# Kernel optimization log

Hardware: AMD Instinct MI355X
Metric: run time of the kernel (lower is better)

Reference implementation:

```python
import jax, jax.numpy as jnp
import numpy as np

TEMPERATURE = 0.07
EPS = 1e-8  # torch CosineSimilarity eps


def setup_inputs() -> dict:
    key = jax.random.key(0)
    k1, k2, k3 = jax.random.split(key, 3)
    N, D = 8192, 512
    features = jax.random.normal(k1, (N, D), dtype=jnp.float32)
    positive_mask = jax.random.randint(k2, (N, N), 0, 2, dtype=jnp.int32)
    negative_mask = jax.random.randint(k3, (N, N), 0, 2, dtype=jnp.int32)
    return {"features": features, "positive_mask": positive_mask, "negative_mask": negative_mask}


def reference(features, positive_mask, negative_mask):
    N = positive_mask.shape[0]
    self_contrast = 1.0 - jnp.eye(N, dtype=features.dtype)  # zero diagonal
    pos = positive_mask.astype(features.dtype) * self_contrast  # [N, N]
    neg = negative_mask.astype(features.dtype) * self_contrast  # [N, N]

    # cosine similarity via normalized matmul (same math as broadcasted CosineSimilarity)
    norm = jnp.maximum(jnp.linalg.norm(features, axis=1, keepdims=True), EPS)
    fn = features / norm  # [N, D]
    sim = jnp.matmul(fn, fn.T) / TEMPERATURE  # [N, N]

    logits_max = jax.lax.stop_gradient(jnp.max(sim, axis=1, keepdims=True))
    e = jnp.exp(sim - logits_max)  # [N, N]

    positives = e * pos
    log_neg_sum = jnp.log(jnp.sum(e * neg, axis=1, keepdims=True))  # [N, 1]
    log_prob = positives - log_neg_sum  # [N, N] (faithful to source: exp-masked, not log)

    cardinal = jnp.sum(pos, axis=1)
    cardinal = jnp.where(cardinal == 0, 1.0, cardinal)
    log_prob_sum = jnp.sum(log_prob * pos, axis=1)
    loss = -log_prob_sum / cardinal
    return jnp.mean(loss)
```

## Files before the change

### kernel.cpp

```cpp
#include <hip/hip_runtime.h>
#include <hip/hip_bf16.h>
#include <math.h>

#define NN 8192
#define DD 512
#define INV_T 14.285714285714286f

typedef __attribute__((ext_vector_type(8))) short s16x8;
typedef __attribute__((ext_vector_type(4))) float f32x4;
typedef __attribute__((ext_vector_type(4))) int   i32x4;

__device__ __forceinline__ unsigned short f32_to_bf16(float f) {
  unsigned int u = __float_as_uint(f);
  u += 0x7FFFu + ((u >> 16) & 1u);
  return (unsigned short)(u >> 16);
}

__device__ __forceinline__ void async16(const void* g, void* l) {
  __builtin_amdgcn_global_load_lds((__attribute__((address_space(1))) void*)(void*)g,
                                   (__attribute__((address_space(3))) void*)l,
                                   16, 0, 0);
}

__global__ __launch_bounds__(256) void normalize_kernel(const float* __restrict__ f,
                                                        unsigned short* __restrict__ fnb) {
  const int wave = threadIdx.x >> 6;
  const int lane = threadIdx.x & 63;
  const int row  = blockIdx.x * 4 + wave;
  const float* src = f + (size_t)row * DD + lane * 8;
  float4 v0 = *(const float4*)src;
  float4 v1 = *(const float4*)(src + 4);
  float ss = v0.x*v0.x + v0.y*v0.y + v0.z*v0.z + v0.w*v0.w
           + v1.x*v1.x + v1.y*v1.y + v1.z*v1.z + v1.w*v1.w;
  #pragma unroll
  for (int o = 32; o; o >>= 1) ss += __shfl_xor(ss, o);
  const float r = 1.0f / fmaxf(sqrtf(ss), 1e-8f);
  ushort4 a, b;
  a.x = f32_to_bf16(v0.x * r); a.y = f32_to_bf16(v0.y * r);
  a.z = f32_to_bf16(v0.z * r); a.w = f32_to_bf16(v0.w * r);
  b.x = f32_to_bf16(v1.x * r); b.y = f32_to_bf16(v1.y * r);
  b.z = f32_to_bf16(v1.z * r); b.w = f32_to_bf16(v1.w * r);
  unsigned short* dst = fnb + (size_t)row * DD + lane * 8;
  *(ushort4*)dst = a;
  *(ushort4*)(dst + 4) = b;
}

__global__ __launch_bounds__(256, 3) void fused_kernel(const unsigned short* __restrict__ fnb,
                                                       const int* __restrict__ posm,
                                                       const int* __restrict__ negm,
                                                       float* __restrict__ Spos,
                                                       float* __restrict__ Sneg,
                                                       float* __restrict__ Pcnt) {
  const int bid = blockIdx.x;
  int bi = (int)(64.5 - sqrt(64.5 * 64.5 - 2.0 * (double)bid));
  while (64 * bi - bi * (bi - 1) / 2 > bid) --bi;
  while (64 * (bi + 1) - (bi + 1) * bi / 2 <= bid) ++bi;
  const int bj = bi + (bid - (64 * bi - bi * (bi - 1) / 2));
  const int I = bi * 128;
  const int J = bj * 128;
  const bool offdiag = (bi != bj);

  const int tid  = threadIdx.x;
  const int wave = tid >> 6;
  const int lane = tid & 63;
  const int wm = wave >> 1;
  const int wn = wave & 1;
  const int q   = lane >> 4;
  const int c16 = lane & 15;

  __shared__ alignas(16) unsigned short lA[128 * 32];
  __shared__ alignas(16) unsigned short lB[128 * 32];
  __shared__ float sacc[2][128][3];
  for (int t = tid; t < 2 * 128 * 3; t += 256) ((float*)sacc)[t] = 0.f;

  f32x4 acc[4][4];
  const f32x4 z4 = {0.f, 0.f, 0.f, 0.f};
  #pragma unroll
  for (int mt = 0; mt < 4; ++mt)
    #pragma unroll
    for (int nt = 0; nt < 4; ++nt) acc[mt][nt] = z4;

  for (int kk = 0; kk < DD / 32; ++kk) {
    const int k0 = kk * 32;
    #pragma unroll
    for (int c = 0; c < 2; ++c) {
      const int fidx = tid + c * 256;
      const int L    = fidx >> 2;
      const int p    = fidx & 3;
      const int csrc = (p ^ ((L >> 1) & 3)) & 3;
      async16(fnb + (size_t)(I + L) * DD + k0 + csrc * 8, (char*)lA + fidx * 16);
      const int gB = 4 * (L & 31) + (L >> 5);
      async16(fnb + (size_t)(J + gB) * DD + k0 + csrc * 8, (char*)lB + fidx * 16);
    }
    __syncthreads();

    s16x8 aF[4], bF[4];
    #pragma unroll
    for (int t = 0; t < 4; ++t) {
      const int arow = wm * 64 + t * 16 + c16;
      const int apos = (q ^ ((arow >> 1) & 3)) & 3;
      aF[t] = *(const s16x8*)((const char*)lA + arow * 64 + apos * 16);
      const int Lb = (wn * 16 + c16) | (t << 5);
      const int bpos = (q ^ ((Lb >> 1) & 3)) & 3;
      bF[t] = *(const s16x8*)((const char*)lB + Lb * 64 + bpos * 16);
    }
    #pragma unroll
    for (int mt = 0; mt < 4; ++mt)
      #pragma unroll
      for (int nt = 0; nt < 4; ++nt)
        acc[mt][nt] = __builtin_amdgcn_mfma_f32_16x16x32_bf16(aF[mt], bF[nt], acc[mt][nt], 0, 0, 0);
    __syncthreads();
  }

  #pragma unroll
  for (int mt = 0; mt < 4; ++mt)
    #pragma unroll
    for (int nt = 0; nt < 4; ++nt)
      #pragma unroll
      for (int r = 0; r < 4; ++r)
        acc[mt][nt][r] = __expf(acc[mt][nt][r] * INV_T - INV_T);

  const bool hasdiag = (bi == bj) && (wm == wn);
  const int cb = wn * 64 + 4 * c16;

  #pragma unroll
  for (int mt = 0; mt < 4; ++mt) {
    const int rl = wm * 64 + mt * 16 + q * 4;
    i32x4 pv[4], nv[4];
    #pragma unroll
    for (int r = 0; r < 4; ++r) {
      const size_t off = (size_t)(I + rl + r) * NN + J + cb;
      pv[r] = __builtin_nontemporal_load((const i32x4*)(posm + off));
      nv[r] = __builtin_nontemporal_load((const i32x4*)(negm + off));
    }
    #pragma unroll
    for (int r = 0; r < 4; ++r) {
      float dsp = 0.f, dsn = 0.f, dpc = 0.f;
      #pragma unroll
      for (int nt = 0; nt < 4; ++nt) {
        float pf = (float)pv[r][nt];
        float nf = (float)nv[r][nt];
        if (hasdiag && (rl + r == cb + nt)) { pf = 0.f; nf = 0.f; }
        const float e = acc[mt][nt][r];
        dsp = fmaf(e, pf, dsp);
        dsn = fmaf(e, nf, dsn);
        dpc += pf;
      }
      #pragma unroll
      for (int o = 1; o <= 8; o <<= 1) {
        dsp += __shfl_xor(dsp, o);
        dsn += __shfl_xor(dsn, o);
        dpc += __shfl_xor(dpc, o);
      }
      if (c16 == 0) {
        atomicAdd(&sacc[0][rl + r][0], dsp);
        atomicAdd(&sacc[0][rl + r][1], dsn);
        atomicAdd(&sacc[0][rl + r][2], dpc);
      }
    }
  }

  if (offdiag) {
    #pragma unroll
    for (int nt = 0; nt < 4; ++nt) {
      const int trl = cb + nt;
      i32x4 pv[4], nv[4];
      #pragma unroll
      for (int mt = 0; mt < 4; ++mt) {
        const size_t off = (size_t)(J + trl) * NN + I + wm * 64 + mt * 16 + q * 4;
        pv[mt] = __builtin_nontemporal_load((const i32x4*)(posm + off));
        nv[mt] = __builtin_nontemporal_load((const i32x4*)(negm + off));
      }
      float ts = 0.f, tn = 0.f, tp = 0.f;
      #pragma unroll
      for (int mt = 0; mt < 4; ++mt) {
        #pragma unroll
        for (int r = 0; r < 4; ++r) {
          const float e = acc[mt][nt][r];
          ts = fmaf(e, (float)pv[mt][r], ts);
          tn = fmaf(e, (float)nv[mt][r], tn);
          tp += (float)pv[mt][r];
        }
      }
      ts += __shfl_xor(ts, 16); ts += __shfl_xor(ts, 32);
      tn += __shfl_xor(tn, 16); tn += __shfl_xor(tn, 32);
      tp += __shfl_xor(tp, 16); tp += __shfl_xor(tp, 32);
      if (q == 0) {
        atomicAdd(&sacc[1][trl][0], ts);
        atomicAdd(&sacc[1][trl][1], tn);
        atomicAdd(&sacc[1][trl][2], tp);
      }
    }
  }

  __syncthreads();

  const int r = tid & 127;
  if (tid < 128) {
    atomicAdd(&Spos[I + r], sacc[0][r][0]);
    atomicAdd(&Sneg[I + r], sacc[0][r][1]);
    atomicAdd(&Pcnt[I + r], sacc[0][r][2]);
  } else if (offdiag) {
    atomicAdd(&Spos[J + r], sacc[1][r][0]);
    atomicAdd(&Sneg[J + r], sacc[1][r][1]);
    atomicAdd(&Pcnt[J + r], sacc[1][r][2]);
  }
}

__global__ __launch_bounds__(256) void finalize_kernel(const float* __restrict__ Spos,
                                                       const float* __restrict__ Sneg,
                                                       const float* __restrict__ Pcnt,
                                                       float* __restrict__ out) {
  float local = 0.f;
  for (int i = threadIdx.x; i < NN; i += 256) {
    const float sp = Spos[i], sn = Sneg[i], pc = Pcnt[i];
    const float card = (pc == 0.f) ? 1.f : pc;
    local += (logf(sn) * pc - sp) / card;
  }
  #pragma unroll
  for (int o = 32; o; o >>= 1) local += __shfl_xor(local, o);
  __shared__ float red[4];
  if ((threadIdx.x & 63) == 0) red[threadIdx.x >> 6] = local;
  __syncthreads();
  if (threadIdx.x == 0)
    out[0] = (red[0] + red[1] + red[2] + red[3]) * (1.0f / (float)NN);
}

extern "C" void kernel_launch(void* const* d_in, const int* in_sizes, int n_in,
                              void* d_out, int out_size, void* d_ws, size_t ws_size,
                              hipStream_t stream) {
  const float* feat = (const float*)d_in[0];
  const int* posm   = (const int*)d_in[1];
  const int* negm   = (const int*)d_in[2];
  float* out = (float*)d_out;

  char* ws = (char*)d_ws;
  unsigned short* fnb = (unsigned short*)ws;
  float* Spos = (float*)(ws + (size_t)8 * 1024 * 1024);
  float* Sneg = Spos + NN;
  float* Pcnt = Sneg + NN;

  hipMemsetAsync(Spos, 0, 3 * NN * sizeof(float), stream);
  normalize_kernel<<<NN / 4, 256, 0, stream>>>(feat, fnb);
  fused_kernel<<<2080, 256, 0, stream>>>(fnb, posm, negm, Spos, Sneg, Pcnt);
  finalize_kernel<<<1, 256, 0, stream>>>(Spos, Sneg, Pcnt, out);
}
```

Measured before the change: 548.2 us.

## Interleave mask loads into the K loop and pack masks as ballot bitmasks

The fused kernel now spreads the positive/negative mask loads across the 16 K iterations of the matmul, using coalesced scalar loads per lane. Each loaded mask is compressed with wave ballots into 64-bit bitmasks in shared memory. The epilogue then reads bits from LDS instead of issuing large vector mask loads after the MFMA loop, so the HBM-bound mask traffic overlaps with compute. Separately, the memset of the accumulators is folded into the normalize kernel to save a launch. The trade-off is extra registers and LDS, plus ballot work inside the main loop.

```diff
diff --git a/kernel.cpp b/kernel.cpp
--- a/kernel.cpp
+++ b/kernel.cpp
@@ -8,7 +8,6 @@
 
 typedef __attribute__((ext_vector_type(8))) short s16x8;
 typedef __attribute__((ext_vector_type(4))) float f32x4;
-typedef __attribute__((ext_vector_type(4))) int   i32x4;
 
 __device__ __forceinline__ unsigned short f32_to_bf16(float f) {
   unsigned int u = __float_as_uint(f);
@@ -23,7 +22,10 @@
 }
 
 __global__ __launch_bounds__(256) void normalize_kernel(const float* __restrict__ f,
-                                                        unsigned short* __restrict__ fnb) {
+                                                        unsigned short* __restrict__ fnb,
+                                                        float* __restrict__ acc) {
+  if (blockIdx.x < 96) acc[blockIdx.x * 256 + threadIdx.x] = 0.f;
+
   const int wave = threadIdx.x >> 6;
   const int lane = threadIdx.x & 63;
   const int row  = blockIdx.x * 4 + wave;
@@ -71,6 +73,7 @@
   __shared__ alignas(16) unsigned short lA[128 * 32];
   __shared__ alignas(16) unsigned short lB[128 * 32];
   __shared__ float sacc[2][128][3];
+  __shared__ unsigned long long pk[4][128][2];
   for (int t = tid; t < 2 * 128 * 3; t += 256) ((float*)sacc)[t] = 0.f;
 
   f32x4 acc[4][4];
@@ -94,6 +97,22 @@
     }
     __syncthreads();
 
+    const int kd    = kk & 3;
+    const int slice = kk >> 2;
+    const bool mact = (kd < 2) || offdiag;
+    int mv[16];
+    if (mact) {
+      const int rbase = (kd & 2) ? J : I;
+      const int cbase = (kd & 2) ? I : J;
+      const int* __restrict__ mp = (kd & 1) ? negm : posm;
+      const int trow0 = slice * 32 + wave * 8;
+      #pragma unroll
+      for (int j = 0; j < 16; ++j) {
+        const int trow = trow0 + (j >> 1);
+        mv[j] = mp[(size_t)(rbase + trow) * NN + cbase + (j & 1) * 64 + lane];
+      }
+    }
+
     s16x8 aF[4], bF[4];
     #pragma unroll
     for (int t = 0; t < 4; ++t) {
@@ -109,6 +128,15 @@
       #pragma unroll
       for (int nt = 0; nt < 4; ++nt)
         acc[mt][nt] = __builtin_amdgcn_mfma_f32_16x16x32_bf16(aF[mt], bF[nt], acc[mt][nt], 0, 0, 0);
+
+    if (mact) {
+      const int trow0 = slice * 32 + wave * 8;
+      #pragma unroll
+      for (int j = 0; j < 16; ++j) {
+        const unsigned long long b = __ballot(mv[j] != 0);
+        if (lane == j) pk[kd][trow0 + (j >> 1)][j & 1] = b;
+      }
+    }
     __syncthreads();
   }
 
@@ -122,25 +150,25 @@
 
   const bool hasdiag = (bi == bj) && (wm == wn);
   const int cb = wn * 64 + 4 * c16;
+  const int half = c16 >> 3;
+  const int bsh  = 4 * (c16 & 7);
 
   #pragma unroll
   for (int mt = 0; mt < 4; ++mt) {
     const int rl = wm * 64 + mt * 16 + q * 4;
-    i32x4 pv[4], nv[4];
     #pragma unroll
     for (int r = 0; r < 4; ++r) {
-      const size_t off = (size_t)(I + rl + r) * NN + J + cb;
-      pv[r] = __builtin_nontemporal_load((const i32x4*)(posm + off));
-      nv[r] = __builtin_nontemporal_load((const i32x4*)(negm + off));
-    }
-    #pragma unroll
-    for (int r = 0; r < 4; ++r) {
+      const int row = rl + r;
+      const uint2 pw = *(const uint2*)&pk[0][row][wn];
+      const uint2 nw = *(const uint2*)&pk[1][row][wn];
+      const unsigned int p32 = half ? pw.y : pw.x;
+      const unsigned int n32 = half ? nw.y : nw.x;
       float dsp = 0.f, dsn = 0.f, dpc = 0.f;
       #pragma unroll
       for (int nt = 0; nt < 4; ++nt) {
-        float pf = (float)pv[r][nt];
-        float nf = (float)nv[r][nt];
-        if (hasdiag && (rl + r == cb + nt)) { pf = 0.f; nf = 0.f; }
+        float pf = (float)((p32 >> (bsh + nt)) & 1u);
+        float nf = (float)((n32 >> (bsh + nt)) & 1u);
+        if (hasdiag && (row == cb + nt)) { pf = 0.f; nf = 0.f; }
         const float e = acc[mt][nt][r];
         dsp = fmaf(e, pf, dsp);
         dsn = fmaf(e, nf, dsn);
@@ -153,9 +181,9 @@
         dpc += __shfl_xor(dpc, o);
       }
       if (c16 == 0) {
-        atomicAdd(&sacc[0][rl + r][0], dsp);
-        atomicAdd(&sacc[0][rl + r][1], dsn);
-        atomicAdd(&sacc[0][rl + r][2], dpc);
+        atomicAdd(&sacc[0][row][0], dsp);
+        atomicAdd(&sacc[0][row][1], dsn);
+        atomicAdd(&sacc[0][row][2], dpc);
       }
     }
   }
@@ -164,22 +192,22 @@
     #pragma unroll
     for (int nt = 0; nt < 4; ++nt) {
       const int trl = cb + nt;
-      i32x4 pv[4], nv[4];
+      const uint2 pw = *(const uint2*)&pk[2][trl][wm];
+      const uint2 nw = *(const uint2*)&pk[3][trl][wm];
+      float ts = 0.f, tn = 0.f, tp = 0.f;
       #pragma unroll
       for (int mt = 0; mt < 4; ++mt) {
-        const size_t off = (size_t)(J + trl) * NN + I + wm * 64 + mt * 16 + q * 4;
-        pv[mt] = __builtin_nontemporal_load((const i32x4*)(posm + off));
-        nv[mt] = __builtin_nontemporal_load((const i32x4*)(negm + off));
-      }
-      float ts = 0.f, tn = 0.f, tp = 0.f;
-      #pragma unroll
-      for (int mt = 0; mt < 4; ++mt) {
+        const unsigned int p32 = (mt < 2) ? pw.x : pw.y;
+        const unsigned int n32 = (mt < 2) ? nw.x : nw.y;
         #pragma unroll
         for (int r = 0; r < 4; ++r) {
+          const int bit = (mt & 1) * 16 + q * 4 + r;
+          const float pf = (float)((p32 >> bit) & 1u);
+          const float nf = (float)((n32 >> bit) & 1u);
           const float e = acc[mt][nt][r];
-          ts = fmaf(e, (float)pv[mt][r], ts);
-          tn = fmaf(e, (float)nv[mt][r], tn);
-          tp += (float)pv[mt][r];
+          ts = fmaf(e, pf, ts);
+          tn = fmaf(e, nf, tn);
+          tp += pf;
         }
       }
       ts += __shfl_xor(ts, 16); ts += __shfl_xor(ts, 32);
@@ -240,8 +268,7 @@
   float* Sneg = Spos + NN;
   float* Pcnt = Sneg + NN;
 
-  hipMemsetAsync(Spos, 0, 3 * NN * sizeof(float), stream);
-  normalize_kernel<<<NN / 4, 256, 0, stream>>>(feat, fnb);
+  normalize_kernel<<<NN / 4, 256, 0, stream>>>(feat, fnb, Spos);
   fused_kernel<<<2080, 256, 0, stream>>>(fnb, posm, negm, Spos, Sneg, Pcnt);
   finalize_kernel<<<1, 256, 0, stream>>>(Spos, Sneg, Pcnt, out);
 }
```

New measurement: 568.6 us. 1.04x slower.

## Double-buffer LDS tiles, remap block order across XCDs, fold memset into normalize

Applied to the files above, without the earlier changes.

The GEMM main loop now double-buffers the A/B LDS tiles, issuing async global-to-LDS loads for the next K slice before computing the current one, so load latency can overlap with MFMA work. Block IDs are permuted so that consecutive triangular tiles are spread in strides of 260, likely to improve per-XCD L2 locality. The separate memset of the accumulators is removed and folded into the normalize kernel. LDS use doubles, which may affect occupancy.

```diff
diff --git a/kernel.cpp b/kernel.cpp
--- a/kernel.cpp
+++ b/kernel.cpp
@@ -23,7 +23,10 @@
 }
 
 __global__ __launch_bounds__(256) void normalize_kernel(const float* __restrict__ f,
-                                                        unsigned short* __restrict__ fnb) {
+                                                        unsigned short* __restrict__ fnb,
+                                                        float* __restrict__ acc) {
+  if (blockIdx.x < 96) acc[blockIdx.x * 256 + threadIdx.x] = 0.f;
+
   const int wave = threadIdx.x >> 6;
   const int lane = threadIdx.x & 63;
   const int row  = blockIdx.x * 4 + wave;
@@ -51,7 +54,7 @@
                                                        float* __restrict__ Spos,
                                                        float* __restrict__ Sneg,
                                                        float* __restrict__ Pcnt) {
-  const int bid = blockIdx.x;
+  const int bid = (blockIdx.x & 7) * 260 + (blockIdx.x >> 3);
   int bi = (int)(64.5 - sqrt(64.5 * 64.5 - 2.0 * (double)bid));
   while (64 * bi - bi * (bi - 1) / 2 > bid) --bi;
   while (64 * (bi + 1) - (bi + 1) * bi / 2 <= bid) ++bi;
@@ -68,8 +71,8 @@
   const int q   = lane >> 4;
   const int c16 = lane & 15;
 
-  __shared__ alignas(16) unsigned short lA[128 * 32];
-  __shared__ alignas(16) unsigned short lB[128 * 32];
+  __shared__ alignas(16) unsigned short lA[2][128 * 32];
+  __shared__ alignas(16) unsigned short lB[2][128 * 32];
   __shared__ float sacc[2][128][3];
   for (int t = tid; t < 2 * 128 * 3; t += 256) ((float*)sacc)[t] = 0.f;
 
@@ -80,36 +83,55 @@
     #pragma unroll
     for (int nt = 0; nt < 4; ++nt) acc[mt][nt] = z4;
 
+  const int fidx0 = tid;
+  #pragma unroll
+  for (int c = 0; c < 2; ++c) {
+    const int fidx = tid + c * 256;
+    const int L    = fidx >> 2;
+    const int p    = fidx & 3;
+    const int csrc = (p ^ ((L >> 1) & 3)) & 3;
+    async16(fnb + (size_t)(I + L) * DD + csrc * 8, (char*)&lA[0][0] + fidx * 16);
+    const int gB = 4 * (L & 31) + (L >> 5);
+    async16(fnb + (size_t)(J + gB) * DD + csrc * 8, (char*)&lB[0][0] + fidx * 16);
+  }
+  __syncthreads();
+
+  int cur = 0;
   for (int kk = 0; kk < DD / 32; ++kk) {
-    const int k0 = kk * 32;
-    #pragma unroll
-    for (int c = 0; c < 2; ++c) {
-      const int fidx = tid + c * 256;
-      const int L    = fidx >> 2;
-      const int p    = fidx & 3;
-      const int csrc = (p ^ ((L >> 1) & 3)) & 3;
-      async16(fnb + (size_t)(I + L) * DD + k0 + csrc * 8, (char*)lA + fidx * 16);
-      const int gB = 4 * (L & 31) + (L >> 5);
-      async16(fnb + (size_t)(J + gB) * DD + k0 + csrc * 8, (char*)lB + fidx * 16);
-    }
-    __syncthreads();
+    if (kk < DD / 32 - 1) {
+      const int k0 = (kk + 1) * 32;
+      const int nb = cur ^ 1;
+      #pragma unroll
+      for (int c = 0; c < 2; ++c) {
+        const int fidx = fidx0 + c * 256;
+        const int L    = fidx >> 2;
+        const int p    = fidx & 3;
+        const int csrc = (p ^ ((L >> 1) & 3)) & 3;
+        async16(fnb + (size_t)(I + L) * DD + k0 + csrc * 8, (char*)&lA[nb][0] + fidx * 16);
+        const int gB = 4 * (L & 31) + (L >> 5);
+        async16(fnb + (size_t)(J + gB) * DD + k0 + csrc * 8, (char*)&lB[nb][0] + fidx * 16);
+      }
+    }
+    __builtin_amdgcn_sched_barrier(0);
 
     s16x8 aF[4], bF[4];
     #pragma unroll
     for (int t = 0; t < 4; ++t) {
       const int arow = wm * 64 + t * 16 + c16;
       const int apos = (q ^ ((arow >> 1) & 3)) & 3;
-      aF[t] = *(const s16x8*)((const char*)lA + arow * 64 + apos * 16);
+      aF[t] = *(const s16x8*)((const char*)&lA[cur][0] + arow * 64 + apos * 16);
       const int Lb = (wn * 16 + c16) | (t << 5);
       const int bpos = (q ^ ((Lb >> 1) & 3)) & 3;
-      bF[t] = *(const s16x8*)((const char*)lB + Lb * 64 + bpos * 16);
+      bF[t] = *(const s16x8*)((const char*)&lB[cur][0] + Lb * 64 + bpos * 16);
     }
     #pragma unroll
     for (int mt = 0; mt < 4; ++mt)
       #pragma unroll
       for (int nt = 0; nt < 4; ++nt)
         acc[mt][nt] = __builtin_amdgcn_mfma_f32_16x16x32_bf16(aF[mt], bF[nt], acc[mt][nt], 0, 0, 0);
+
     __syncthreads();
+    cur ^= 1;
   }
 
   #pragma unroll
@@ -240,8 +262,7 @@
   float* Sneg = Spos + NN;
   float* Pcnt = Sneg + NN;
 
-  hipMemsetAsync(Spos, 0, 3 * NN * sizeof(float), stream);
-  normalize_kernel<<<NN / 4, 256, 0, stream>>>(feat, fnb);
+  normalize_kernel<<<NN / 4, 256, 0, stream>>>(feat, fnb, Spos);
   fused_kernel<<<2080, 256, 0, stream>>>(fnb, posm, negm, Spos, Sneg, Pcnt);
   finalize_kernel<<<1, 256, 0, stream>>>(Spos, Sneg, Pcnt, out);
 }
```

Measured after the change: 545.6 us (median of 3 runs). Within noise of the previous version (-0.5%).

## Triple-buffer K tiles with async LDS loads, remap blocks, fold memset into normalize

Applied to the files above, without the earlier changes.

The GEMM K loop now uses three LDS buffers, prefetching two tiles ahead with global_load_lds and explicit vmcnt waits, so loads overlap the MFMA work instead of being fully serialized. Block IDs are permuted across groups of 8, which likely spreads triangular tiles across XCDs for better L2 locality. The separate hipMemsetAsync is replaced by zeroing the accumulators inside normalize_kernel. In exchange, LDS use triples, which may lower occupancy, and the hand-written waitcnt logic depends on an exact count of outstanding loads.

```diff
diff --git a/kernel.cpp b/kernel.cpp
--- a/kernel.cpp
+++ b/kernel.cpp
@@ -23,7 +23,10 @@
 }
 
 __global__ __launch_bounds__(256) void normalize_kernel(const float* __restrict__ f,
-                                                        unsigned short* __restrict__ fnb) {
+                                                        unsigned short* __restrict__ fnb,
+                                                        float* __restrict__ acc) {
+  if (blockIdx.x < 96) acc[blockIdx.x * 256 + threadIdx.x] = 0.f;
+
   const int wave = threadIdx.x >> 6;
   const int lane = threadIdx.x & 63;
   const int row  = blockIdx.x * 4 + wave;
@@ -51,7 +54,7 @@
                                                        float* __restrict__ Spos,
                                                        float* __restrict__ Sneg,
                                                        float* __restrict__ Pcnt) {
-  const int bid = blockIdx.x;
+  const int bid = (blockIdx.x & 7) * 260 + (blockIdx.x >> 3);
   int bi = (int)(64.5 - sqrt(64.5 * 64.5 - 2.0 * (double)bid));
   while (64 * bi - bi * (bi - 1) / 2 > bid) --bi;
   while (64 * (bi + 1) - (bi + 1) * bi / 2 <= bid) ++bi;
@@ -68,8 +71,8 @@
   const int q   = lane >> 4;
   const int c16 = lane & 15;
 
-  __shared__ alignas(16) unsigned short lA[128 * 32];
-  __shared__ alignas(16) unsigned short lB[128 * 32];
+  __shared__ alignas(16) unsigned short lA[3][128 * 32];
+  __shared__ alignas(16) unsigned short lB[3][128 * 32];
   __shared__ float sacc[2][128][3];
   for (int t = tid; t < 2 * 128 * 3; t += 256) ((float*)sacc)[t] = 0.f;
 
@@ -80,37 +83,64 @@
     #pragma unroll
     for (int nt = 0; nt < 4; ++nt) acc[mt][nt] = z4;
 
+  #define STAGE_TILE(kt, buf)                                                   \
+    do {                                                                        \
+      const int _k0 = (kt) * 32;                                                \
+      _Pragma("unroll")                                                         \
+      for (int _c = 0; _c < 2; ++_c) {                                          \
+        const int _fidx = tid + _c * 256;                                       \
+        const int _L    = _fidx >> 2;                                           \
+        const int _p    = _fidx & 3;                                            \
+        const int _csrc = (_p ^ ((_L >> 1) & 3)) & 3;                           \
+        async16(fnb + (size_t)(I + _L) * DD + _k0 + _csrc * 8,                  \
+                (char*)&lA[(buf)][0] + _fidx * 16);                             \
+        const int _gB = 4 * (_L & 31) + (_L >> 5);                              \
+        async16(fnb + (size_t)(J + _gB) * DD + _k0 + _csrc * 8,                 \
+                (char*)&lB[(buf)][0] + _fidx * 16);                             \
+      }                                                                         \
+    } while (0)
+
+  STAGE_TILE(0, 0);
+  STAGE_TILE(1, 1);
+
+  int cb = 0;
+  int sb = 2;
   for (int kk = 0; kk < DD / 32; ++kk) {
-    const int k0 = kk * 32;
-    #pragma unroll
-    for (int c = 0; c < 2; ++c) {
-      const int fidx = tid + c * 256;
-      const int L    = fidx >> 2;
-      const int p    = fidx & 3;
-      const int csrc = (p ^ ((L >> 1) & 3)) & 3;
-      async16(fnb + (size_t)(I + L) * DD + k0 + csrc * 8, (char*)lA + fidx * 16);
-      const int gB = 4 * (L & 31) + (L >> 5);
-      async16(fnb + (size_t)(J + gB) * DD + k0 + csrc * 8, (char*)lB + fidx * 16);
-    }
-    __syncthreads();
-
+    if (kk + 2 < DD / 32) STAGE_TILE(kk + 2, sb);
+    __builtin_amdgcn_sched_barrier(0);
+    if (kk + 2 < DD / 32)      asm volatile("s_waitcnt vmcnt(8)" ::: "memory");
+    else if (kk + 1 < DD / 32) asm volatile("s_waitcnt vmcnt(4)" ::: "memory");
+    else                       asm volatile("s_waitcnt vmcnt(0)" ::: "memory");
+    __builtin_amdgcn_sched_barrier(0);
+    __builtin_amdgcn_s_barrier();
+    __builtin_amdgcn_sched_barrier(0);
+
+    const char* bA = (const char*)&lA[cb][0];
+    const char* bB = (const char*)&lB[cb][0];
     s16x8 aF[4], bF[4];
     #pragma unroll
     for (int t = 0; t < 4; ++t) {
       const int arow = wm * 64 + t * 16 + c16;
       const int apos = (q ^ ((arow >> 1) & 3)) & 3;
-      aF[t] = *(const s16x8*)((const char*)lA + arow * 64 + apos * 16);
+      aF[t] = *(const s16x8*)(bA + arow * 64 + apos * 16);
       const int Lb = (wn * 16 + c16) | (t << 5);
       const int bpos = (q ^ ((Lb >> 1) & 3)) & 3;
-      bF[t] = *(const s16x8*)((const char*)lB + Lb * 64 + bpos * 16);
+      bF[t] = *(const s16x8*)(bB + Lb * 64 + bpos * 16);
     }
     #pragma unroll
     for (int mt = 0; mt < 4; ++mt)
       #pragma unroll
       for (int nt = 0; nt < 4; ++nt)
         acc[mt][nt] = __builtin_amdgcn_mfma_f32_16x16x32_bf16(aF[mt], bF[nt], acc[mt][nt], 0, 0, 0);
-    __syncthreads();
-  }
+
+    __builtin_amdgcn_sched_barrier(0);
+    __builtin_amdgcn_s_barrier();
+    __builtin_amdgcn_sched_barrier(0);
+
+    cb = (cb == 2) ? 0 : cb + 1;
+    sb = (sb == 2) ? 0 : sb + 1;
+  }
+  #undef STAGE_TILE
 
   #pragma unroll
   for (int mt = 0; mt < 4; ++mt)
@@ -121,7 +151,7 @@
         acc[mt][nt][r] = __expf(acc[mt][nt][r] * INV_T - INV_T);
 
   const bool hasdiag = (bi == bj) && (wm == wn);
-  const int cb = wn * 64 + 4 * c16;
+  const int cb2 = wn * 64 + 4 * c16;
 
   #pragma unroll
   for (int mt = 0; mt < 4; ++mt) {
@@ -129,7 +159,7 @@
     i32x4 pv[4], nv[4];
     #pragma unroll
     for (int r = 0; r < 4; ++r) {
-      const size_t off = (size_t)(I + rl + r) * NN + J + cb;
+      const size_t off = (size_t)(I + rl + r) * NN + J + cb2;
       pv[r] = __builtin_nontemporal_load((const i32x4*)(posm + off));
       nv[r] = __builtin_nontemporal_load((const i32x4*)(negm + off));
     }
@@ -140,7 +170,7 @@
       for (int nt = 0; nt < 4; ++nt) {
         float pf = (float)pv[r][nt];
         float nf = (float)nv[r][nt];
-        if (hasdiag && (rl + r == cb + nt)) { pf = 0.f; nf = 0.f; }
+        if (hasdiag && (rl + r == cb2 + nt)) { pf = 0.f; nf = 0.f; }
         const float e = acc[mt][nt][r];
         dsp = fmaf(e, pf, dsp);
         dsn = fmaf(e, nf, dsn);
@@ -163,7 +193,7 @@
   if (offdiag) {
     #pragma unroll
     for (int nt = 0; nt < 4; ++nt) {
-      const int trl = cb + nt;
+      const int trl = cb2 + nt;
       i32x4 pv[4], nv[4];
       #pragma unroll
       for (int mt = 0; mt < 4; ++mt) {
@@ -240,8 +270,7 @@
   float* Sneg = Spos + NN;
   float* Pcnt = Sneg + NN;
 
-  hipMemsetAsync(Spos, 0, 3 * NN * sizeof(float), stream);
-  normalize_kernel<<<NN / 4, 256, 0, stream>>>(feat, fnb);
+  normalize_kernel<<<NN / 4, 256, 0, stream>>>(feat, fnb, Spos);
   fused_kernel<<<2080, 256, 0, stream>>>(fnb, posm, negm, Spos, Sneg, Pcnt);
   finalize_kernel<<<1, 256, 0, stream>>>(Spos, Sneg, Pcnt, out);
 }
```

New measurement: 549.4 us. Within noise of the previous version (+0.2%).
